# Optimization experiments

Measured on AMD Instinct MI355X. Metric: run time of the kernel, lower is better.

Reference implementation:

```python
import jax, jax.numpy as jnp
import numpy as np

H = 4; HID = 128; NEG = 0.2
N_GEN, N_BUS, N_RES = 50000, 80000, 10000
N = N_GEN + N_BUS + N_RES
E_PROD, E_SERV, E_TRAN, E_BACK = 100000, 100000, 150000, 50000


def _lrelu(x):
    return jnp.where(x >= 0, x, NEG * x)


def _heat_layer(x, src, dst, node_type, edge_type, edge_attr, hW, hb, ete, eae, attw, linw):
    # HeteroLinear: x @ W[node_type] + b[node_type] (compute for all 3 types, select)
    xt = jnp.einsum('nd,tdo->nto', x, hW)                                  # [N,3,HID]
    x = jnp.take_along_axis(xt, node_type[:, None, None], axis=1)[:, 0, :] + hb[node_type]
    etee = _lrelu(ete[edge_type])                                          # [E,16]
    eaee = _lrelu(edge_attr @ eae)                                         # [E,16]
    x_i = x[dst]                                                           # target nodes
    x_j = x[src]                                                           # source nodes
    a = _lrelu(jnp.concatenate([x_i, x_j, etee, eaee], axis=-1) @ attw)    # [E,H]
    # softmax over incoming edges of each target node (PyG softmax: eps=1e-16)
    m = jax.ops.segment_max(a, dst, num_segments=N)                        # [N,H]
    a = jnp.exp(a - m[dst])
    denom = jax.ops.segment_sum(a, dst, num_segments=N)
    alpha = a / (denom[dst] + 1e-16)                                       # [E,H]
    msg = jnp.concatenate([x_j, eaee], axis=-1) @ linw                     # [E,HID]
    # concat=False -> mean over heads of alpha[:,h,None]*msg; fold the head
    # mean into alpha to avoid the [E,H,HID] intermediate (identical math).
    return jax.ops.segment_sum(msg * alpha.mean(axis=-1, keepdims=True), dst, num_segments=N)


def _forward(x_gen, x_bus, x_res, ea_prod, ea_served, ea_trans, ea_backed,
             pW_gen, pb_gen, pW_bus, pb_bus, pW_res, pb_res,
             hW1, hb1, ete1, eae1, attw1, linw1,
             hW2, hb2, ete2, eae2, attw2, linw2,
             hW3, hb3, ete3, eae3, attw3, linw3,
             ei_prod, ei_served, ei_trans, ei_backed):
    x = jnp.concatenate([x_gen @ pW_gen + pb_gen,
                         x_bus @ pW_bus + pb_bus,
                         x_res @ pW_res + pb_res], axis=0)                  # [N,HID]
    node_type = jnp.concatenate([jnp.full((N_GEN,), 0, jnp.int32),
                                 jnp.full((N_BUS,), 1, jnp.int32),
                                 jnp.full((N_RES,), 2, jnp.int32)])
    ei = jnp.concatenate([ei_prod, ei_served, ei_trans, ei_backed], axis=1)
    src, dst = ei[0], ei[1]
    edge_attr = jnp.concatenate([ea_prod, ea_served, ea_trans, ea_backed], axis=0)
    edge_type = jnp.concatenate([jnp.full((E_PROD,), 0, jnp.int32),
                                 jnp.full((E_SERV,), 1, jnp.int32),
                                 jnp.full((E_TRAN,), 2, jnp.int32),
                                 jnp.full((E_BACK,), 3, jnp.int32)])
    x1 = jax.nn.relu(_heat_layer(x, src, dst, node_type, edge_type, edge_attr,
                                 hW1, hb1, ete1, eae1, attw1, linw1))
    x2 = jax.nn.relu(_heat_layer(x1, src, dst, node_type, edge_type, edge_attr,
                                 hW2, hb2, ete2, eae2, attw2, linw2)) + x1
    x3 = jax.nn.relu(_heat_layer(x2, src, dst, node_type, edge_type, edge_attr,
                                 hW3, hb3, ete3, eae3, attw3, linw3)) + x2
    return x3  # dropout is identity in eval mode


def setup_inputs() -> dict:
    key = jax.random.key(0)
    ks = iter(jax.random.split(key, 64))

    def nrm(shape, s=0.05):
        return jax.random.normal(next(ks), shape, jnp.float32) * s

    def eidx(n_e, slo, shi, dlo, dhi):
        s = jax.random.randint(next(ks), (n_e,), slo, shi, dtype=jnp.int32)
        d = jax.random.randint(next(ks), (n_e,), dlo, dhi, dtype=jnp.int32)
        return jnp.stack([s, d], axis=0)

    inp = {
        'x_gen': nrm((N_GEN, 39), 1.0),
        'x_bus': nrm((N_BUS, 16), 1.0),
        'x_res': nrm((N_RES, 16), 1.0),
        'ei_prod': eidx(E_PROD, 0, N_GEN, N_GEN, N_GEN + N_BUS),
        'ei_served': eidx(E_SERV, N_GEN, N_GEN + N_BUS, 0, N_GEN),
        'ei_trans': eidx(E_TRAN, N_GEN, N_GEN + N_BUS, N_GEN, N_GEN + N_BUS),
        'ei_backed': eidx(E_BACK, N_GEN + N_BUS, N, 0, N_GEN),
        'ea_prod': nrm((E_PROD, 2), 1.0),
        'ea_served': nrm((E_SERV, 2), 1.0),
        'ea_trans': nrm((E_TRAN, 2), 1.0),
        'ea_backed': nrm((E_BACK, 2), 1.0),
        'pW_gen': nrm((39, HID)), 'pb_gen': nrm((HID,)),
        'pW_bus': nrm((16, HID)), 'pb_bus': nrm((HID,)),
        'pW_res': nrm((16, HID)), 'pb_res': nrm((HID,)),
    }
    for l in (1, 2, 3):
        inp[f'hW{l}'] = nrm((3, HID, HID))
        inp[f'hb{l}'] = nrm((3, HID))
        inp[f'ete{l}'] = nrm((4, 16))
        inp[f'eae{l}'] = nrm((2, 16))
        inp[f'attw{l}'] = nrm((2 * HID + 16 + 16, H))
        inp[f'linw{l}'] = nrm((HID + 16, HID))
    return inp


def reference(x_gen, x_bus, x_res, ei_prod, ei_served, ei_trans, ei_backed,
              ea_prod, ea_served, ea_trans, ea_backed,
              pW_gen, pb_gen, pW_bus, pb_bus, pW_res, pb_res,
              hW1, hb1, ete1, eae1, attw1, linw1,
              hW2, hb2, ete2, eae2, attw2, linw2,
              hW3, hb3, ete3, eae3, attw3, linw3):
    return _forward(x_gen, x_bus, x_res, ea_prod, ea_served, ea_trans, ea_backed,
                    pW_gen, pb_gen, pW_bus, pb_bus, pW_res, pb_res,
                    hW1, hb1, ete1, eae1, attw1, linw1,
                    hW2, hb2, ete2, eae2, attw2, linw2,
                    hW3, hb3, ete3, eae3, attw3, linw3,
                    ei_prod, ei_served, ei_trans, ei_backed)
```

## Files before the change

kernel.cpp:

```cpp
#include <hip/hip_runtime.h>
#include <hip/hip_bf16.h>

#define NGEN 50000
#define NBUS 80000
#define NRES 10000
#define NTOT 140000
#define EPROD 100000
#define ESERV 100000
#define ETRAN 150000
#define EBACK 50000
#define ETOT  400000
#define HID 128
#define NEGS 0.2f

#define NB_SCAN 547
#define EB 1563
#define WB 35000
#define NW16 8750
#define PGRID 768
#define HGRID 1024
#define AGGW 160
#define LINP 172
#define HETP 140

typedef __attribute__((ext_vector_type(8))) short bf16x8;
typedef __attribute__((ext_vector_type(8))) unsigned short u16x8;
typedef __attribute__((ext_vector_type(4))) float f32x4;

__device__ __forceinline__ float lrelu(float x) { return x >= 0.f ? x : NEGS * x; }
__device__ __forceinline__ float b2f(ushort u) { union { float f; uint i; } v; v.i = (uint)u << 16; return v.f; }
__device__ __forceinline__ ushort f2b(float f) {
  union { float f; uint i; } v; v.f = f;
  return (ushort)((v.i + 0x7FFF + ((v.i >> 16) & 1)) >> 16);
}

__global__ __launch_bounds__(256) void k_setup_edges(
    const int* __restrict__ eip, const int* __restrict__ eis,
    const int* __restrict__ eit, const int* __restrict__ eib,
    const float* __restrict__ eap, const float* __restrict__ eas,
    const float* __restrict__ eat, const float* __restrict__ eab,
    int* __restrict__ esrc, int* __restrict__ edst, float* __restrict__ ea_all,
    int* __restrict__ cnt)
{
  int e = blockIdx.x * 256 + threadIdx.x;
  if (e >= ETOT) return;
  int s, d; float a0, a1;
  if (e < EPROD) { s = eip[e]; d = eip[EPROD + e]; a0 = eap[2*e]; a1 = eap[2*e+1]; }
  else if (e < EPROD+ESERV) { int i = e - EPROD; s = eis[i]; d = eis[ESERV + i]; a0 = eas[2*i]; a1 = eas[2*i+1]; }
  else if (e < EPROD+ESERV+ETRAN) { int i = e - EPROD - ESERV; s = eit[i]; d = eit[ETRAN + i]; a0 = eat[2*i]; a1 = eat[2*i+1]; }
  else { int i = e - EPROD - ESERV - ETRAN; s = eib[i]; d = eib[EBACK + i]; a0 = eab[2*i]; a1 = eab[2*i+1]; }
  esrc[e] = s; edst[e] = d; ea_all[2*e] = a0; ea_all[2*e+1] = a1;
  atomicAdd(&cnt[d], 1);
}

__global__ __launch_bounds__(256) void k_scan1(const int* __restrict__ cnt,
                                               int* __restrict__ rp, int* __restrict__ bsum)
{
  int t = threadIdx.x, i = blockIdx.x * 256 + t;
  int v = (i < NTOT) ? cnt[i] : 0;
  __shared__ int buf[256];
  buf[t] = v; __syncthreads();
  for (int off = 1; off < 256; off <<= 1) {
    int x = (t >= off) ? buf[t - off] : 0;
    __syncthreads(); buf[t] += x; __syncthreads();
  }
  if (i < NTOT) rp[i] = buf[t] - v;
  if (t == 255) bsum[blockIdx.x] = buf[255];
}

__global__ __launch_bounds__(1024) void k_scan2(int* __restrict__ bsum, int nb)
{
  int t = threadIdx.x;
  __shared__ int buf[1024];
  int v = (t < nb) ? bsum[t] : 0;
  buf[t] = v; __syncthreads();
  for (int off = 1; off < 1024; off <<= 1) {
    int x = (t >= off) ? buf[t - off] : 0;
    __syncthreads(); buf[t] += x; __syncthreads();
  }
  if (t < nb) bsum[t] = buf[t] - v;
}

__global__ __launch_bounds__(256) void k_scan3(int* __restrict__ rp, const int* __restrict__ bsum)
{
  int i = blockIdx.x * 256 + threadIdx.x;
  if (i < NTOT) rp[i] += bsum[blockIdx.x];
  if (i == 0) rp[NTOT] = ETOT;
}

__global__ __launch_bounds__(256) void k_scatter(const int* __restrict__ esrc,
    const int* __restrict__ edst, const int* __restrict__ rp,
    int* __restrict__ fill, int2* __restrict__ plist)
{
  int e = blockIdx.x * 256 + threadIdx.x;
  if (e >= ETOT) return;
  int d = edst[e];
  int pos = rp[d] + atomicAdd(&fill[d], 1);
  plist[pos] = make_int2(esrc[e], e);
}

__global__ __launch_bounds__(256) void k_convW(
    const float* __restrict__ pg, const float* __restrict__ pb, const float* __restrict__ pr,
    const float* __restrict__ h1, const float* __restrict__ l1,
    const float* __restrict__ h2, const float* __restrict__ l2,
    const float* __restrict__ h3, const float* __restrict__ l3,
    ushort* __restrict__ dst)
{
  int idx = blockIdx.x * 256 + threadIdx.x;
  if (idx >= 233472) return;
  const float* src; int K, KP, base;
  if (idx < 24576) {
    int s = idx >> 13;
    src = (s == 0) ? pg : (s == 1) ? pb : pr;
    K = (s == 0) ? 39 : 16; KP = 64; base = s * 8192;
  } else {
    int r = idx - 24576, l = r / 69632, q = r % 69632;
    const float* h = (l == 0) ? h1 : (l == 1) ? h2 : h3;
    const float* lw = (l == 0) ? l1 : (l == 1) ? l2 : l3;
    if (q < 49152) { int t = q >> 14; src = h + t * 16384; K = 128; KP = 128; base = 24576 + l * 69632 + t * 16384; }
    else { src = lw; K = 144; KP = 160; base = 24576 + l * 69632 + 49152; }
  }
  int li = idx - base, c = li / KP, k = li % KP;
  dst[idx] = (k < K) ? f2b(src[k * 128 + c]) : (ushort)0;
}

struct Seg {
  const void* A; const ushort* Wt; const float* bias;
  int lda, K, M, nb, rbase;
};

__global__ __launch_bounds__(256) void k_mgemm3(Seg s0, Seg s1, Seg s2, int KP, ushort* __restrict__ Cb)
{
  __shared__ ushort As[128][72];
  __shared__ ushort Bs[128][72];
  int bid = blockIdx.x;
  Seg sg = s0;
  if (bid >= s0.nb + s1.nb) { sg = s2; bid -= s0.nb + s1.nb; }
  else if (bid >= s0.nb) { sg = s1; bid -= s0.nb; }

  const int tid = threadIdx.x;
  const int lr = tid & 15, hi = (tid & 63) >> 4;
  const int w = tid >> 6;
  const int wrow = (w >> 1) * 64, wcol = (w & 1) * 64;
  const int brow = bid * 128;

  f32x4 acc[4][4];
#pragma unroll
  for (int m = 0; m < 4; ++m)
#pragma unroll
    for (int n = 0; n < 4; ++n) acc[m][n] = (f32x4){0.f, 0.f, 0.f, 0.f};

  for (int k0 = 0; k0 < KP; k0 += 64) {
#pragma unroll
    for (int p = 0; p < 8; ++p) {
      int li = tid + 256 * p;
      int row = li >> 4, c4 = (li & 15) * 4;
      int gr = brow + row, gk = k0 + c4;
      ushort4 u = make_ushort4(0, 0, 0, 0);
      if (gr < sg.M) {
        const float* A = (const float*)sg.A;
        const float* ar = A + (size_t)gr * sg.lda;
        if (gk + 0 < sg.K) u.x = f2b(ar[gk + 0]);
        if (gk + 1 < sg.K) u.y = f2b(ar[gk + 1]);
        if (gk + 2 < sg.K) u.z = f2b(ar[gk + 2]);
        if (gk + 3 < sg.K) u.w = f2b(ar[gk + 3]);
      }
      *(ushort4*)&As[row][c4] = u;
    }
#pragma unroll
    for (int p = 0; p < 8; ++p) {
      int li = tid + 256 * p;
      int row = li >> 4, c4 = (li & 15) * 4;
      *(ushort4*)&Bs[row][c4] = *(const ushort4*)&sg.Wt[(size_t)row * KP + k0 + c4];
    }
    __syncthreads();
#pragma unroll
    for (int kk = 0; kk < 64; kk += 32) {
      bf16x8 af[4], bfv[4];
#pragma unroll
      for (int m = 0; m < 4; ++m) af[m] = *(const bf16x8*)&As[wrow + m * 16 + lr][kk + hi * 8];
#pragma unroll
      for (int n = 0; n < 4; ++n) bfv[n] = *(const bf16x8*)&Bs[wcol + n * 16 + lr][kk + hi * 8];
#pragma unroll
      for (int m = 0; m < 4; ++m)
#pragma unroll
        for (int n = 0; n < 4; ++n)
          acc[m][n] = __builtin_amdgcn_mfma_f32_16x16x32_bf16(af[m], bfv[n], acc[m][n], 0, 0, 0);
    }
    __syncthreads();
  }

#pragma unroll
  for (int m = 0; m < 4; ++m) {
#pragma unroll
    for (int j = 0; j < 4; ++j) {
      int gr = brow + wrow + m * 16 + hi * 4 + j;
      if (gr >= sg.M) continue;
#pragma unroll
      for (int n = 0; n < 4; ++n) {
        int col = wcol + n * 16 + lr;
        float v = acc[m][n][j] + sg.bias[col];
        Cb[(size_t)(sg.rbase + gr) * 128 + col] = f2b(v);
      }
    }
  }
}

__global__ __launch_bounds__(256) void k_wgemm_het(
    const ushort* __restrict__ A,
    const ushort* __restrict__ WtH,
    const float* __restrict__ hb,
    const float* __restrict__ attw,
    ushort* __restrict__ xh,
    float* __restrict__ sd, float* __restrict__ ss)
{
  __shared__ ushort Ws[128 * HETP];
  __shared__ float atw[1152];
  const int tid = threadIdx.x;
  const int bid = blockIdx.x;
  int seg, lb, nb, ntile, segbase, segrows;
  if (bid < 366)      { seg = 0; lb = bid;       nb = 366; ntile = 782;  segbase = 0;           segrows = NGEN; }
  else if (bid < 951) { seg = 1; lb = bid - 366; nb = 585; ntile = 1250; segbase = NGEN;        segrows = NBUS; }
  else                { seg = 2; lb = bid - 951; nb = 73;  ntile = 157;  segbase = NGEN + NBUS; segrows = NRES; }

  const int w = tid >> 6;
  const int lane = tid & 63;
  const int lr = lane & 15, hi = lane >> 4;

  int t = lb;
  int rl = t * 64 + w * 16;
  int valid = rl < segrows;
  int r0 = segbase + (valid ? rl : 0);
  {
    const ushort* Ap = A + (size_t)(r0 + lr) * 128 + hi * 8;
    __builtin_prefetch(Ap, 0, 0);
  }
  const ushort* Ar0 = A + (size_t)(r0 + lr) * 128 + hi * 8;
  bf16x8 a0 = *(const bf16x8*)(Ar0);
  bf16x8 a1 = *(const bf16x8*)(Ar0 + 32);
  bf16x8 a2 = *(const bf16x8*)(Ar0 + 64);
  bf16x8 a3 = *(const bf16x8*)(Ar0 + 96);

  {
    const ushort* src = WtH + seg * 16384 + tid * 64;
    ushort* dstl = Ws + (tid >> 1) * HETP + (tid & 1) * 64;
#pragma unroll
    for (int j = 0; j < 8; ++j)
      *(u16x8*)&dstl[j * 8] = *(const u16x8*)&src[j * 8];
    for (int i = tid; i < 1152; i += 256) atw[i] = attw[i];
  }
  __syncthreads();

  const float* bias = hb + seg * 128;

  for (; t < ntile; t += nb) {
    const int curvalid = valid, currow = r0;
    bf16x8 c0 = a0, c1 = a1, c2 = a2, c3 = a3;
    int tn = t + nb;
    if (tn < ntile) {
      rl = tn * 64 + w * 16;
      valid = rl < segrows;
      r0 = segbase + (valid ? rl : 0);
      const ushort* An = A + (size_t)(r0 + lr) * 128 + hi * 8;
      a0 = *(const bf16x8*)(An);
      a1 = *(const bf16x8*)(An + 32);
      a2 = *(const bf16x8*)(An + 64);
      a3 = *(const bf16x8*)(An + 96);
    }
    if (!curvalid) continue;

    f32x4 acc[8];
#pragma unroll
    for (int n = 0; n < 8; ++n) acc[n] = (f32x4){0.f, 0.f, 0.f, 0.f};
    const ushort* wb0 = Ws + lr * HETP + hi * 8;
#pragma unroll
    for (int n = 0; n < 8; ++n) {
      const ushort* wn = wb0 + n * 16 * HETP;
      acc[n] = __builtin_amdgcn_mfma_f32_16x16x32_bf16(*(const bf16x8*)(wn),      c0, acc[n], 0, 0, 0);
      acc[n] = __builtin_amdgcn_mfma_f32_16x16x32_bf16(*(const bf16x8*)(wn + 32), c1, acc[n], 0, 0, 0);
      acc[n] = __builtin_amdgcn_mfma_f32_16x16x32_bf16(*(const bf16x8*)(wn + 64), c2, acc[n], 0, 0, 0);
      acc[n] = __builtin_amdgcn_mfma_f32_16x16x32_bf16(*(const bf16x8*)(wn + 96), c3, acc[n], 0, 0, 0);
    }

    const int row = currow + lr;
    float pd0 = 0.f, pd1 = 0.f, pd2 = 0.f, pd3 = 0.f;
    float ps0 = 0.f, ps1 = 0.f, ps2 = 0.f, ps3 = 0.f;
#pragma unroll
    for (int n = 0; n < 8; ++n) {
      int c0i = n * 16 + hi * 4;
      float4 bv = *(const float4*)&bias[c0i];
      f32x4 v = acc[n];
      v[0] += bv.x; v[1] += bv.y; v[2] += bv.z; v[3] += bv.w;
      *(ushort4*)&xh[(size_t)row * 128 + c0i] = make_ushort4(f2b(v[0]), f2b(v[1]), f2b(v[2]), f2b(v[3]));
#pragma unroll
      for (int j = 0; j < 4; ++j) {
        float4 wd = *(const float4*)&atw[(c0i + j) * 4];
        float4 ws = *(const float4*)&atw[(128 + c0i + j) * 4];
        pd0 += v[j] * wd.x; pd1 += v[j] * wd.y; pd2 += v[j] * wd.z; pd3 += v[j] * wd.w;
        ps0 += v[j] * ws.x; ps1 += v[j] * ws.y; ps2 += v[j] * ws.z; ps3 += v[j] * ws.w;
      }
    }
    pd0 += __shfl_xor(pd0, 16); pd0 += __shfl_xor(pd0, 32);
    pd1 += __shfl_xor(pd1, 16); pd1 += __shfl_xor(pd1, 32);
    pd2 += __shfl_xor(pd2, 16); pd2 += __shfl_xor(pd2, 32);
    pd3 += __shfl_xor(pd3, 16); pd3 += __shfl_xor(pd3, 32);
    ps0 += __shfl_xor(ps0, 16); ps0 += __shfl_xor(ps0, 32);
    ps1 += __shfl_xor(ps1, 16); ps1 += __shfl_xor(ps1, 32);
    ps2 += __shfl_xor(ps2, 16); ps2 += __shfl_xor(ps2, 32);
    ps3 += __shfl_xor(ps3, 16); ps3 += __shfl_xor(ps3, 32);
    if (hi == 0) {
      float4 o = {pd0, pd1, pd2, pd3};
      *(float4*)&sd[row * 4] = o;
    } else if (hi == 1) {
      float4 o = {ps0, ps1, ps2, ps3};
      *(float4*)&ss[row * 4] = o;
    }
  }
}

template<int HASRES, int LAST>
__global__ __launch_bounds__(256) void k_wgemm_lin(
    const ushort* __restrict__ A,
    const ushort* __restrict__ Wt,
    const ushort* residb,
    float* __restrict__ Cf,
    ushort* Cb)
{
  __shared__ ushort Ws[128 * LINP];
  const int tid = threadIdx.x;
  const int lane = tid & 63;
  const int lr = lane & 15, hi = lane >> 4;
  const int w = tid >> 6;

  int gw = blockIdx.x * 4 + w;
  {
    const ushort* Ar0 = A + (size_t)(gw * 16 + lr) * AGGW + hi * 8;
    __builtin_prefetch(Ar0, 0, 0);
  }
  const ushort* Ar0 = A + (size_t)(gw * 16 + lr) * AGGW + hi * 8;
  bf16x8 a0 = *(const bf16x8*)(Ar0);
  bf16x8 a1 = *(const bf16x8*)(Ar0 + 32);
  bf16x8 a2 = *(const bf16x8*)(Ar0 + 64);
  bf16x8 a3 = *(const bf16x8*)(Ar0 + 96);
  bf16x8 a4 = *(const bf16x8*)(Ar0 + 128);

  {
    const ushort* src = Wt + tid * 80;
    ushort* dstl = Ws + (tid >> 1) * LINP + (tid & 1) * 80;
#pragma unroll
    for (int j = 0; j < 10; ++j)
      *(u16x8*)&dstl[j * 8] = *(const u16x8*)&src[j * 8];
  }
  __syncthreads();

  for (; gw < NW16; gw += PGRID * 4) {
    const int gcur = gw;
    bf16x8 c0 = a0, c1 = a1, c2 = a2, c3 = a3, c4 = a4;
    int gn = gw + PGRID * 4;
    if (gn < NW16) {
      const ushort* An = A + (size_t)(gn * 16 + lr) * AGGW + hi * 8;
      a0 = *(const bf16x8*)(An);
      a1 = *(const bf16x8*)(An + 32);
      a2 = *(const bf16x8*)(An + 64);
      a3 = *(const bf16x8*)(An + 96);
      a4 = *(const bf16x8*)(An + 128);
    }

    f32x4 acc[8];
#pragma unroll
    for (int n = 0; n < 8; ++n) acc[n] = (f32x4){0.f, 0.f, 0.f, 0.f};
    const ushort* wb0 = Ws + lr * LINP + hi * 8;
#pragma unroll
    for (int n = 0; n < 8; ++n) {
      const ushort* wn = wb0 + n * 16 * LINP;
      acc[n] = __builtin_amdgcn_mfma_f32_16x16x32_bf16(*(const bf16x8*)(wn),       c0, acc[n], 0, 0, 0);
      acc[n] = __builtin_amdgcn_mfma_f32_16x16x32_bf16(*(const bf16x8*)(wn + 32),  c1, acc[n], 0, 0, 0);
      acc[n] = __builtin_amdgcn_mfma_f32_16x16x32_bf16(*(const bf16x8*)(wn + 64),  c2, acc[n], 0, 0, 0);
      acc[n] = __builtin_amdgcn_mfma_f32_16x16x32_bf16(*(const bf16x8*)(wn + 96),  c3, acc[n], 0, 0, 0);
      acc[n] = __builtin_amdgcn_mfma_f32_16x16x32_bf16(*(const bf16x8*)(wn + 128), c4, acc[n], 0, 0, 0);
    }

    const int row = gcur * 16 + lr;
#pragma unroll
    for (int n = 0; n < 8; ++n) {
      int c0i = n * 16 + hi * 4;
      f32x4 v = acc[n];
      v[0] = fmaxf(v[0], 0.f); v[1] = fmaxf(v[1], 0.f);
      v[2] = fmaxf(v[2], 0.f); v[3] = fmaxf(v[3], 0.f);
      if (HASRES) {
        ushort4 r = *(const ushort4*)&residb[(size_t)row * 128 + c0i];
        v[0] += b2f(r.x); v[1] += b2f(r.y); v[2] += b2f(r.z); v[3] += b2f(r.w);
      }
      if (LAST) {
        *(f32x4*)&Cf[(size_t)row * 128 + c0i] = v;
      } else {
        *(ushort4*)&Cb[(size_t)row * 128 + c0i] =
            make_ushort4(f2b(v[0]), f2b(v[1]), f2b(v[2]), f2b(v[3]));
      }
    }
  }
}

__global__ __launch_bounds__(256) void k_edge(
    const int* __restrict__ esrc, const int* __restrict__ edst,
    const float* __restrict__ ea_all, const float* __restrict__ eae,
    const float* __restrict__ attw, const float* __restrict__ ete,
    const float* __restrict__ sd, const float* __restrict__ ss,
    ushort* __restrict__ eaeeB, float* __restrict__ a4buf)
{
  __shared__ float tc[4][4];
  if (threadIdx.x < 16) {
    int tt = threadIdx.x >> 2, h = threadIdx.x & 3;
    float s = 0.f;
    for (int j = 0; j < 16; ++j) s += lrelu(ete[tt * 16 + j]) * attw[(256 + j) * 4 + h];
    tc[tt][h] = s;
  }
  __syncthreads();

  int e = blockIdx.x * 256 + threadIdx.x;
  if (e >= ETOT) return;
  int t = (e < EPROD) ? 0 : (e < EPROD + ESERV) ? 1 : (e < EPROD + ESERV + ETRAN) ? 2 : 3;
  float a0 = ea_all[2 * e], a1 = ea_all[2 * e + 1];
  int s = esrc[e], d = edst[e];
  float4 sdv = *(const float4*)&sd[d * 4];
  float4 ssv = *(const float4*)&ss[s * 4];
  float acc[4] = {sdv.x + ssv.x + tc[t][0], sdv.y + ssv.y + tc[t][1],
                  sdv.z + ssv.z + tc[t][2], sdv.w + ssv.w + tc[t][3]};
  ushort us[16];
#pragma unroll
  for (int j = 0; j < 16; ++j) {
    float v = lrelu(a0 * eae[j] + a1 * eae[16 + j]);
    us[j] = f2b(v);
    float4 aw = *(const float4*)&attw[(272 + j) * 4];
    acc[0] += v * aw.x; acc[1] += v * aw.y; acc[2] += v * aw.z; acc[3] += v * aw.w;
  }
  *(ushort4*)&eaeeB[(size_t)e * 16 + 0]  = make_ushort4(us[0], us[1], us[2], us[3]);
  *(ushort4*)&eaeeB[(size_t)e * 16 + 4]  = make_ushort4(us[4], us[5], us[6], us[7]);
  *(ushort4*)&eaeeB[(size_t)e * 16 + 8]  = make_ushort4(us[8], us[9], us[10], us[11]);
  *(ushort4*)&eaeeB[(size_t)e * 16 + 12] = make_ushort4(us[12], us[13], us[14], us[15]);
  float4 out = {lrelu(acc[0]), lrelu(acc[1]), lrelu(acc[2]), lrelu(acc[3])};
  *(float4*)&a4buf[e * 4] = out;
}

__global__ __launch_bounds__(256) void k_softmax(
    const int* __restrict__ rp, const int2* __restrict__ plist,
    const float* __restrict__ a4buf, float* __restrict__ ab)
{
  int n = blockIdx.x * 256 + threadIdx.x;
  if (n >= NTOT) return;
  int beg = rp[n], end = rp[n + 1];
  if (beg == end) return;
  float m0 = -INFINITY, m1 = -INFINITY, m2 = -INFINITY, m3 = -INFINITY;
  for (int i = beg; i < end; ++i) {
    int e = plist[i].y;
    float4 av = *(const float4*)&a4buf[(size_t)e * 4];
    m0 = fmaxf(m0, av.x); m1 = fmaxf(m1, av.y); m2 = fmaxf(m2, av.z); m3 = fmaxf(m3, av.w);
  }
  float d0 = 0.f, d1 = 0.f, d2 = 0.f, d3 = 0.f;
  for (int i = beg; i < end; ++i) {
    int e = plist[i].y;
    float4 av = *(const float4*)&a4buf[(size_t)e * 4];
    d0 += __expf(av.x - m0); d1 += __expf(av.y - m1);
    d2 += __expf(av.z - m2); d3 += __expf(av.w - m3);
  }
  d0 = 1.f / (d0 + 1e-16f); d1 = 1.f / (d1 + 1e-16f);
  d2 = 1.f / (d2 + 1e-16f); d3 = 1.f / (d3 + 1e-16f);
  for (int i = beg; i < end; ++i) {
    int e = plist[i].y;
    float4 av = *(const float4*)&a4buf[(size_t)e * 4];
    ab[i] = 0.25f * (__expf(av.x - m0) * d0 + __expf(av.y - m1) * d1 +
                     __expf(av.z - m2) * d2 + __expf(av.w - m3) * d3);
  }
}

__global__ __launch_bounds__(256) void k_gather(
    const int* __restrict__ rp, const int2* __restrict__ plist,
    const float* __restrict__ ab, const ushort* __restrict__ eaeeB,
    const ushort* __restrict__ xh, ushort* __restrict__ agg)
{
  int wid = (blockIdx.x * 256 + threadIdx.x) >> 6;
  int lane = threadIdx.x & 63;
  if (wid >= NTOT) return;
  int beg = rp[wid], end = rp[wid + 1];
  const int l2 = lane & 31;
  const int half = lane >> 5;

  f32x4 axv = (f32x4){0.f, 0.f, 0.f, 0.f};
  float ae0 = 0.f, ae1 = 0.f;

  for (int i = beg; i < end; i += 2) {
    int idx = i + half;
    bool valid = idx < end;
    int idc = valid ? idx : beg;
    int2 pe = plist[idc];
    float w = valid ? ab[idc] : 0.f;
    ushort4 xv = *(const ushort4*)&xh[(size_t)pe.x * 128 + l2 * 4];
    axv[0] += w * b2f(xv.x); axv[1] += w * b2f(xv.y);
    axv[2] += w * b2f(xv.z); axv[3] += w * b2f(xv.w);
    if (l2 < 8) {
      ushort2 q = *(const ushort2*)&eaeeB[(size_t)pe.y * 16 + l2 * 2];
      ae0 += w * b2f(q.x); ae1 += w * b2f(q.y);
    }
  }
#pragma unroll
  for (int j = 0; j < 4; ++j) axv[j] += __shfl_xor(axv[j], 32);
  ae0 += __shfl_xor(ae0, 32); ae1 += __shfl_xor(ae1, 32);

  size_t rb = (size_t)wid * AGGW;
  if (half == 0) {
    *(ushort4*)&agg[rb + l2 * 4] =
        make_ushort4(f2b(axv[0]), f2b(axv[1]), f2b(axv[2]), f2b(axv[3]));
  } else {
    if (l2 < 8) *(ushort2*)&agg[rb + 128 + l2 * 2] = make_ushort2(f2b(ae0), f2b(ae1));
    else if (l2 < 16) *(ushort2*)&agg[rb + 144 + (l2 - 8) * 2] = make_ushort2(0, 0);
  }
}

extern "C" void kernel_launch(void* const* d_in, const int* in_sizes, int n_in,
                              void* d_out, int out_size, void* d_ws, size_t ws_size,
                              hipStream_t stream)
{
  const float* x_gen = (const float*)d_in[0];
  const float* x_bus = (const float*)d_in[1];
  const float* x_res = (const float*)d_in[2];
  const int* eip = (const int*)d_in[3];
  const int* eis = (const int*)d_in[4];
  const int* eit = (const int*)d_in[5];
  const int* eib = (const int*)d_in[6];
  const float* eap = (const float*)d_in[7];
  const float* eas = (const float*)d_in[8];
  const float* eat = (const float*)d_in[9];
  const float* eab = (const float*)d_in[10];
  const float* pW_gen = (const float*)d_in[11];
  const float* pb_gen = (const float*)d_in[12];
  const float* pW_bus = (const float*)d_in[13];
  const float* pb_bus = (const float*)d_in[14];
  const float* pW_res = (const float*)d_in[15];
  const float* pb_res = (const float*)d_in[16];

  float* out = (float*)d_out;

  char* p = (char*)d_ws;
  auto alloc = [&](size_t bytes) -> void* {
    void* r = (void*)p;
    p += (bytes + 255) & ~(size_t)255;
    return r;
  };
  int* esrc    = (int*)alloc((size_t)ETOT * 4);
  int* edst    = (int*)alloc((size_t)ETOT * 4);
  float* ea_all = (float*)alloc((size_t)ETOT * 2 * 4);
  int* cnt     = (int*)alloc((size_t)NTOT * 4);
  int* fill    = (int*)alloc((size_t)NTOT * 4);
  int* rp      = (int*)alloc((size_t)(NTOT + 1) * 4);
  int* bsum    = (int*)alloc(1024 * 4);
  int2* plist  = (int2*)alloc((size_t)ETOT * 8);
  float* ab    = (float*)alloc((size_t)ETOT * 4);
  ushort* Wt   = (ushort*)alloc((size_t)233472 * 2);
  ushort* x_bf = (ushort*)alloc((size_t)NTOT * HID * 2);
  ushort* xh_bf = (ushort*)alloc((size_t)NTOT * HID * 2);
  float* sd    = (float*)alloc((size_t)NTOT * 4 * 4);
  float* ss    = (float*)alloc((size_t)NTOT * 4 * 4);
  ushort* eaeeB = (ushort*)alloc((size_t)ETOT * 16 * 2);
  float* a4buf = (float*)alloc((size_t)ETOT * 4 * 4);
  ushort* agg  = (ushort*)alloc((size_t)NTOT * AGGW * 2);

  hipMemsetAsync(cnt, 0, (size_t)NTOT * 4, stream);
  hipMemsetAsync(fill, 0, (size_t)NTOT * 4, stream);
  k_setup_edges<<<EB, 256, 0, stream>>>(eip, eis, eit, eib, eap, eas, eat, eab, esrc, edst, ea_all, cnt);
  k_scan1<<<NB_SCAN, 256, 0, stream>>>(cnt, rp, bsum);
  k_scan2<<<1, 1024, 0, stream>>>(bsum, NB_SCAN);
  k_scan3<<<NB_SCAN, 256, 0, stream>>>(rp, bsum);
  k_scatter<<<EB, 256, 0, stream>>>(esrc, edst, rp, fill, plist);

  k_convW<<<912, 256, 0, stream>>>(pW_gen, pW_bus, pW_res,
      (const float*)d_in[17], (const float*)d_in[22],
      (const float*)d_in[23], (const float*)d_in[28],
      (const float*)d_in[29], (const float*)d_in[34], Wt);

  const int NB0 = (NGEN + 127) / 128, NB1 = (NBUS + 127) / 128, NB2 = (NRES + 127) / 128;
  const int NBT = NB0 + NB1 + NB2;

  {
    Seg s0{x_gen, Wt + 0,     pb_gen, 39, 39, NGEN, NB0, 0};
    Seg s1{x_bus, Wt + 8192,  pb_bus, 16, 16, NBUS, NB1, NGEN};
    Seg s2{x_res, Wt + 16384, pb_res, 16, 16, NRES, NB2, NGEN + NBUS};
    k_mgemm3<<<NBT, 256, 0, stream>>>(s0, s1, s2, 64, x_bf);
  }

  for (int l = 0; l < 3; ++l) {
    const float* hb   = (const float*)d_in[18 + l * 6];
    const float* ete  = (const float*)d_in[19 + l * 6];
    const float* eae  = (const float*)d_in[20 + l * 6];
    const float* attw = (const float*)d_in[21 + l * 6];
    const ushort* WtH = Wt + 24576 + l * 69632;
    const ushort* WtL = Wt + 24576 + l * 69632 + 49152;

    k_wgemm_het<<<HGRID, 256, 0, stream>>>(x_bf, WtH, hb, attw, xh_bf, sd, ss);

    k_edge<<<EB, 256, 0, stream>>>(esrc, edst, ea_all, eae, attw, ete, sd, ss, eaeeB, a4buf);
    k_softmax<<<NB_SCAN, 256, 0, stream>>>(rp, plist, a4buf, ab);
    k_gather<<<WB, 256, 0, stream>>>(rp, plist, ab, eaeeB, xh_bf, agg);

    if (l == 0)      k_wgemm_lin<0,0><<<PGRID, 256, 0, stream>>>(agg, WtL, nullptr, nullptr, x_bf);
    else if (l == 1) k_wgemm_lin<1,0><<<PGRID, 256, 0, stream>>>(agg, WtL, x_bf, nullptr, x_bf);
    else             k_wgemm_lin<1,1><<<PGRID, 256, 0, stream>>>(agg, WtL, x_bf, out, nullptr);
  }
}
```

Baseline: 626.2 us.

## Shrink het GEMM grid, read attention weights from global, add empty-node gather early exit

The heterogeneous-linear GEMM now launches 768 blocks instead of 1024, with the per-segment block split rebalanced to match. It drops the shared-memory copy of the attention weights and reads them directly from global memory. The explicit prefetch hints in both GEMM kernels are removed. The gather kernel gains an early exit that zero-fills the aggregation row for nodes with no incoming edges, skipping the edge loop and shuffles for those nodes. Together these aim to cut launch and LDS overhead, at the risk of less latency hiding and slower uncached-looking global reads of the attention weights.

Result: faster. 587.5 us (-6.2%).

```diff
diff --git a/kernel.cpp b/kernel.cpp
--- a/kernel.cpp
+++ b/kernel.cpp
@@ -18,7 +18,6 @@
 #define WB 35000
 #define NW16 8750
 #define PGRID 768
-#define HGRID 1024
 #define AGGW 160
 #define LINP 172
 #define HETP 140
@@ -215,31 +214,25 @@
     float* __restrict__ sd, float* __restrict__ ss)
 {
   __shared__ ushort Ws[128 * HETP];
-  __shared__ float atw[1152];
   const int tid = threadIdx.x;
   const int bid = blockIdx.x;
   int seg, lb, nb, ntile, segbase, segrows;
-  if (bid < 366)      { seg = 0; lb = bid;       nb = 366; ntile = 782;  segbase = 0;           segrows = NGEN; }
-  else if (bid < 951) { seg = 1; lb = bid - 366; nb = 585; ntile = 1250; segbase = NGEN;        segrows = NBUS; }
-  else                { seg = 2; lb = bid - 951; nb = 73;  ntile = 157;  segbase = NGEN + NBUS; segrows = NRES; }
+  if (bid < 274)      { seg = 0; lb = bid;       nb = 274; ntile = 782;  segbase = 0;           segrows = NGEN; }
+  else if (bid < 712) { seg = 1; lb = bid - 274; nb = 438; ntile = 1250; segbase = NGEN;        segrows = NBUS; }
+  else                { seg = 2; lb = bid - 712; nb = 56;  ntile = 157;  segbase = NGEN + NBUS; segrows = NRES; }
 
   const int w = tid >> 6;
   const int lane = tid & 63;
   const int lr = lane & 15, hi = lane >> 4;
 
-  int t = lb;
-  int rl = t * 64 + w * 16;
+  int rl = lb * 64 + w * 16;
   int valid = rl < segrows;
   int r0 = segbase + (valid ? rl : 0);
-  {
-    const ushort* Ap = A + (size_t)(r0 + lr) * 128 + hi * 8;
-    __builtin_prefetch(Ap, 0, 0);
-  }
-  const ushort* Ar0 = A + (size_t)(r0 + lr) * 128 + hi * 8;
-  bf16x8 a0 = *(const bf16x8*)(Ar0);
-  bf16x8 a1 = *(const bf16x8*)(Ar0 + 32);
-  bf16x8 a2 = *(const bf16x8*)(Ar0 + 64);
-  bf16x8 a3 = *(const bf16x8*)(Ar0 + 96);
+  const ushort* Ap = A + (size_t)(r0 + lr) * 128 + hi * 8;
+  bf16x8 a0 = *(const bf16x8*)(Ap);
+  bf16x8 a1 = *(const bf16x8*)(Ap + 32);
+  bf16x8 a2 = *(const bf16x8*)(Ap + 64);
+  bf16x8 a3 = *(const bf16x8*)(Ap + 96);
 
   {
     const ushort* src = WtH + seg * 16384 + tid * 64;
@@ -247,15 +240,15 @@
 #pragma unroll
     for (int j = 0; j < 8; ++j)
       *(u16x8*)&dstl[j * 8] = *(const u16x8*)&src[j * 8];
-    for (int i = tid; i < 1152; i += 256) atw[i] = attw[i];
   }
   __syncthreads();
 
   const float* bias = hb + seg * 128;
 
-  for (; t < ntile; t += nb) {
+  for (int t = lb; t < ntile; t += nb) {
     const int curvalid = valid, currow = r0;
     bf16x8 c0 = a0, c1 = a1, c2 = a2, c3 = a3;
+
     int tn = t + nb;
     if (tn < ntile) {
       rl = tn * 64 + w * 16;
@@ -294,8 +287,8 @@
       *(ushort4*)&xh[(size_t)row * 128 + c0i] = make_ushort4(f2b(v[0]), f2b(v[1]), f2b(v[2]), f2b(v[3]));
 #pragma unroll
       for (int j = 0; j < 4; ++j) {
-        float4 wd = *(const float4*)&atw[(c0i + j) * 4];
-        float4 ws = *(const float4*)&atw[(128 + c0i + j) * 4];
+        float4 wd = *(const float4*)&attw[(c0i + j) * 4];
+        float4 ws = *(const float4*)&attw[(128 + c0i + j) * 4];
         pd0 += v[j] * wd.x; pd1 += v[j] * wd.y; pd2 += v[j] * wd.z; pd3 += v[j] * wd.w;
         ps0 += v[j] * ws.x; ps1 += v[j] * ws.y; ps2 += v[j] * ws.z; ps3 += v[j] * ws.w;
       }
@@ -333,10 +326,6 @@
   const int w = tid >> 6;
 
   int gw = blockIdx.x * 4 + w;
-  {
-    const ushort* Ar0 = A + (size_t)(gw * 16 + lr) * AGGW + hi * 8;
-    __builtin_prefetch(Ar0, 0, 0);
-  }
   const ushort* Ar0 = A + (size_t)(gw * 16 + lr) * AGGW + hi * 8;
   bf16x8 a0 = *(const bf16x8*)(Ar0);
   bf16x8 a1 = *(const bf16x8*)(Ar0 + 32);
@@ -484,6 +473,13 @@
   int beg = rp[wid], end = rp[wid + 1];
   const int l2 = lane & 31;
   const int half = lane >> 5;
+  size_t rb = (size_t)wid * AGGW;
+
+  if (beg == end) {
+    *(ushort2*)&agg[rb + lane * 2] = make_ushort2(0, 0);
+    if (lane < 16) *(ushort2*)&agg[rb + 128 + lane * 2] = make_ushort2(0, 0);
+    return;
+  }
 
   f32x4 axv = (f32x4){0.f, 0.f, 0.f, 0.f};
   float ae0 = 0.f, ae1 = 0.f;
@@ -506,7 +502,6 @@
   for (int j = 0; j < 4; ++j) axv[j] += __shfl_xor(axv[j], 32);
   ae0 += __shfl_xor(ae0, 32); ae1 += __shfl_xor(ae1, 32);
 
-  size_t rb = (size_t)wid * AGGW;
   if (half == 0) {
     *(ushort4*)&agg[rb + l2 * 4] =
         make_ushort4(f2b(axv[0]), f2b(axv[1]), f2b(axv[2]), f2b(axv[3]));
@@ -595,7 +590,7 @@
     const ushort* WtH = Wt + 24576 + l * 69632;
     const ushort* WtL = Wt + 24576 + l * 69632 + 49152;
 
-    k_wgemm_het<<<HGRID, 256, 0, stream>>>(x_bf, WtH, hb, attw, xh_bf, sd, ss);
+    k_wgemm_het<<<PGRID, 256, 0, stream>>>(x_bf, WtH, hb, attw, xh_bf, sd, ss);
 
     k_edge<<<EB, 256, 0, stream>>>(esrc, edst, ea_all, eae, attw, ete, sd, ss, eaeeB, a4buf);
     k_softmax<<<NB_SCAN, 256, 0, stream>>>(rp, plist, a4buf, ab);
```
